# Optimization experiments

Hardware: AMD Instinct MI355X
Metric: run time of the kernel (lower is better)

The kernel has to match this reference:

```python
import jax, jax.numpy as jnp
import numpy as np

MARGIN = 0.1  # init kwarg: margin
# type_of_distance='euclidean', type_of_quadruplets='hard', what_is_hard='one'


def _distance_euclidean(x):
    # l2-normalize rows, then all-pairs euclidean distance (torch.cdist p=2)
    x = x / jnp.linalg.norm(x, axis=1, keepdims=True)
    sq = jnp.sum(x * x, axis=1)
    d2 = sq[:, None] + sq[None, :] - 2.0 * (x @ x.T)
    return jnp.sqrt(jnp.maximum(d2, 0.0))


def setup_inputs() -> dict:
    key = jax.random.key(0)
    k1, k2 = jax.random.split(key)
    B, D, C = 256, 512, 80
    logits = jax.random.normal(k1, (B, D), dtype=jnp.float32)
    # sparse multi-hot labels: ~2.4 active classes per sample
    labels = (jax.random.uniform(k2, (B, C)) < 0.03).astype(jnp.float32)
    return {"logits": logits, "labels": labels}


def reference(logits, labels):
    n = labels.shape[0]
    sames = (labels @ labels.T) > 0                      # [B,B] bool
    diffs = ~sames
    sames = sames & ~jnp.eye(n, dtype=bool)              # fill_diagonal_(0)
    triu = jnp.triu(jnp.ones((n, n), dtype=bool), k=1)   # J < K
    # O(B^3) quadruplet-candidate mask: sames[I,J] & sames[I,K] & (J<K)
    mask = sames[:, :, None] & sames[:, None, :] & triu[None, :, :]
    I, J, K = jnp.nonzero(mask)                          # row-major, same as torch.where
    # expand each (I,J,K) triplet with every negative N of anchor I
    rows, cols = jnp.nonzero(diffs[I])                   # [n_quads]
    quadruplets = jnp.stack([I[rows], J[rows], K[rows], cols], axis=1)

    mat = _distance_euclidean(jax.lax.stop_gradient(logits))  # logits.detach()
    Ii, Jj, Kk, Nn = quadruplets[:, 0], quadruplets[:, 1], quadruplets[:, 2], quadruplets[:, 3]
    ij = mat[Ii, Jj]
    ik = mat[Ii, Kk]
    innd = mat[Ii, Nn]
    m1 = innd - ij
    m2 = innd - ik
    # type_of_quadruplets='hard', what_is_hard='one' (opt = OR)
    cond = ((m1 <= MARGIN) | (m2 <= MARGIN)) & ((m1 <= 0) | (m2 <= 0))
    return quadruplets[cond]
```

## Files before the change

### kernel.cpp

```cpp
#include <hip/hip_runtime.h>
#include <math.h>

#define NB 256
#define ND 512
#define NC 80
#define NSPLIT 8
#define SLOT 32640
#define KW_WAVES (NB * NSPLIT * 4)

__device__ float g_x [NB * ND];
__device__ float g_xt[ND * NB];
__device__ float g_sq[NB];
__device__ float g_ddneg[NB * NB];
__device__ unsigned long long g_m[NB * 2];
__device__ int   g_atot[NB];
__device__ int   g_abase[NB];
__device__ int   g_cursor;
__device__ int4  g_trip[NB * SLOT];

__device__ __forceinline__ int block_scan_int(int val, int* wsum) {
    int tid = threadIdx.x, wv = tid >> 6, ln = tid & 63;
    int v = val;
    #pragma unroll
    for (int off = 1; off < 64; off <<= 1) {
        int u = __shfl_up(v, off);
        v += (ln >= off) ? u : 0;
    }
    __syncthreads();
    if (ln == 63) wsum[wv] = v;
    __syncthreads();
    int add = 0;
    #pragma unroll
    for (int w = 0; w < 4; ++w) if (w < wv) add += wsum[w];
    return v + add;
}

__device__ __forceinline__ int ubcount(const float* s, float thr) {
    int pos = 0;
    #pragma unroll
    for (int step = 128; step > 0; step >>= 1) {
        int np = pos + step;
        if (s[np - 1] <= thr) pos = np;
    }
    return pos;
}

__global__ __launch_bounds__(256) void k_prep(const float* __restrict__ logits,
                                              const float* __restrict__ labels) {
    int b = blockIdx.x, tid = threadIdx.x;
    __shared__ double red[NB];
    if (b == 0 && tid == 0) g_cursor = 0;
    float v0 = logits[b * ND + tid];
    float v1 = logits[b * ND + 256 + tid];
    red[tid] = (double)(v0 * v0) + (double)(v1 * v1);
    __syncthreads();
    for (int off = 128; off > 0; off >>= 1) {
        if (tid < off) red[tid] += red[tid + off];
        __syncthreads();
    }
    float S = (float)red[0];
    float nrm = sqrtf(S);
    __syncthreads();
    float a0 = v0 / nrm;
    float a1 = v1 / nrm;
    g_x[b * ND + tid]          = a0;
    g_x[b * ND + 256 + tid]    = a1;
    g_xt[tid * NB + b]         = a0;
    g_xt[(tid + 256) * NB + b] = a1;
    red[tid] = (double)(a0 * a0) + (double)(a1 * a1);
    __syncthreads();
    for (int off = 128; off > 0; off >>= 1) {
        if (tid < off) red[tid] += red[tid + off];
        __syncthreads();
    }
    if (tid == 0) g_sq[b] = (float)red[0];
    int wv = tid >> 6, ln = tid & 63;
    if (wv == 0) {
        unsigned long long m0 = __ballot(labels[b * NC + ln] != 0.0f);
        if (ln == 0) g_m[2 * b] = m0;
    } else if (wv == 1) {
        bool p = (ln < 16) ? (labels[b * NC + 64 + ln] != 0.0f) : false;
        unsigned long long m1 = __ballot(p);
        if (ln == 0) g_m[2 * b + 1] = m1;
    }
}

__global__ __launch_bounds__(256) void k_count() {
    __shared__ float xi[ND];
    __shared__ float s_dd[NB], s_sort[NB];
    __shared__ int s_w4[4], s_rowbase[NB], s_base;
    __shared__ short s_plist[NB];
    int i = blockIdx.x, tid = threadIdx.x;
    xi[tid]       = g_x[i * ND + tid];
    xi[tid + 256] = g_x[i * ND + 256 + tid];
    __syncthreads();
    double dot = 0.0;
    #pragma unroll 8
    for (int c = 0; c < ND; ++c)
        dot = fma((double)xi[c], (double)g_xt[c * NB + tid], dot);
    float dotf = (float)dot;
    float sm   = g_sq[i] + g_sq[tid];
    float d2   = sm - 2.0f * dotf;
    float dv   = sqrtf(d2 > 0.0f ? d2 : 0.0f);
    s_dd[tid] = dv;
    unsigned long long mi0 = g_m[2 * i],   mi1 = g_m[2 * i + 1];
    unsigned long long mt0 = g_m[2 * tid], mt1 = g_m[2 * tid + 1];
    bool shl   = ((mi0 & mt0) | (mi1 & mt1)) != 0ULL;
    bool isPos = shl && (tid != i);
    float ddneg = shl ? INFINITY : dv;
    g_ddneg[i * NB + tid] = ddneg;
    int incl = block_scan_int(isPos ? 1 : 0, s_w4);
    int P = s_w4[0] + s_w4[1] + s_w4[2] + s_w4[3];
    if (isPos) s_plist[incl - 1] = (short)tid;
    if (tid < P - 1) s_rowbase[tid] = tid * (P - 1) - (tid * (tid - 1)) / 2;
    float v = ddneg;
    for (int k = 2; k <= 256; k <<= 1)
        for (int j = k >> 1; j > 0; j >>= 1) {
            float oth;
            if (j >= 64) {
                __syncthreads();
                s_sort[tid] = v;
                __syncthreads();
                oth = s_sort[tid ^ j];
            } else {
                oth = __shfl_xor(v, j);
            }
            bool keepmin = (((tid & k) == 0) == ((tid & j) == 0));
            v = keepmin ? fminf(v, oth) : fmaxf(v, oth);
        }
    __syncthreads();
    s_sort[tid] = v;
    int T = P * (P - 1) / 2;
    if (tid == 0) s_base = (T > 0) ? atomicAdd(&g_cursor, T) : 0;
    __syncthreads();
    int dbase = s_base;
    int carried = 0;
    for (int cb = 0; cb < T; cb += NB) {
        int t = cb + tid;
        int cnt = 0, jk = 0;
        float thr = 0.0f;
        if (t < T) {
            int a = 0;
            #pragma unroll
            for (int step = 128; step > 0; step >>= 1) {
                int na = a + step;
                if (na <= P - 2 && s_rowbase[na] <= t) a = na;
            }
            int b = a + 1 + (t - s_rowbase[a]);
            int jj = s_plist[a], kk = s_plist[b];
            thr = fmaxf(s_dd[jj], s_dd[kk]);
            jk  = jj | (kk << 8);
            cnt = ubcount(s_sort, thr);
        }
        int inc2 = block_scan_int(cnt, s_w4);
        int chunkTot = s_w4[0] + s_w4[1] + s_w4[2] + s_w4[3];
        if (t < T)
            g_trip[dbase + t] =
                make_int4(jk, __float_as_int(thr), carried + inc2 - cnt, i);
        carried += chunkTot;
    }
    if (tid == 0) g_atot[i] = carried;
}

__global__ __launch_bounds__(256) void k_abase() {
    __shared__ int s_w4[4];
    int tid = threadIdx.x;
    int v = g_atot[tid];
    int incl = block_scan_int(v, s_w4);
    g_abase[tid] = incl - v;
}

__global__ __launch_bounds__(256) void k_write(int4* __restrict__ out, int maxQuads) {
    int tid = threadIdx.x;
    int wv = tid >> 6, ln = tid & 63;
    int W = (blockIdx.x << 2) | wv;
    int Ttot = g_cursor;
    unsigned long long lanemask = (1ULL << ln) - 1ULL;
    int t = W;
    int4 tr = (t < Ttot) ? g_trip[t] : make_int4(0, 0, 0, 0);
    while (t < Ttot) {
        int tn = t + KW_WAVES;
        int4 nxt = (tn < Ttot) ? g_trip[tn] : make_int4(0, 0, 0, 0);
        int ai = tr.w;
        const float* row = g_ddneg + ai * NB;
        float v0 = row[ln], v1 = row[64 + ln];
        float v2 = row[128 + ln], v3 = row[192 + ln];
        int base = g_abase[ai] + tr.z;
        int jj = tr.x & 255, kk = tr.x >> 8;
        float thr = __int_as_float(tr.y);
        bool f0 = (v0 <= thr), f1 = (v1 <= thr);
        bool f2 = (v2 <= thr), f3 = (v3 <= thr);
        unsigned long long m0 = __ballot(f0), m1 = __ballot(f1);
        unsigned long long m2 = __ballot(f2), m3 = __ballot(f3);
        int b1 = base + __popcll(m0);
        int b2 = b1 + __popcll(m1);
        int b3 = b2 + __popcll(m2);
        if (f0) { int pos = base + __popcll(m0 & lanemask);
                  if (pos < maxQuads) out[pos] = make_int4(ai, jj, kk, ln); }
        if (f1) { int pos = b1 + __popcll(m1 & lanemask);
                  if (pos < maxQuads) out[pos] = make_int4(ai, jj, kk, 64 | ln); }
        if (f2) { int pos = b2 + __popcll(m2 & lanemask);
                  if (pos < maxQuads) out[pos] = make_int4(ai, jj, kk, 128 | ln); }
        if (f3) { int pos = b3 + __popcll(m3 & lanemask);
                  if (pos < maxQuads) out[pos] = make_int4(ai, jj, kk, 192 | ln); }
        tr = nxt;
        t = tn;
    }
}

extern "C" void kernel_launch(void* const* d_in, const int* in_sizes, int n_in,
                              void* d_out, int out_size, void* d_ws, size_t ws_size,
                              hipStream_t stream) {
    const float* logits = (const float*)d_in[0];
    const float* labels = (const float*)d_in[1];
    if (n_in >= 2 && in_sizes[0] == NB * NC && in_sizes[1] == NB * ND) {
        logits = (const float*)d_in[1];
        labels = (const float*)d_in[0];
    }
    int maxQuads = out_size / 4;

    k_prep <<<NB, NB, 0, stream>>>(logits, labels);
    k_count<<<NB, NB, 0, stream>>>();
    k_abase<<<1,  NB, 0, stream>>>();
    k_write<<<NB * NSPLIT, NB, 0, stream>>>((int4*)d_out, maxQuads);
}
```

Baseline: 187.2 us.

## Fuse anchor-base scan into write kernel and process contiguous triplet chunks per wave

Removes the separate k_abase launch: each k_write block redoes the 256-entry prefix scan of per-anchor totals into shared memory. Each wave now takes a contiguous range of triplets instead of a strided one. It loads 64 triplets with one coalesced read and broadcasts them via shuffles, and reloads the anchor's negative-distance row only when the anchor changes. This cuts a launch, redundant row loads and scattered triplet reads. The cost is a redundant scan in every block and more serialized per-triplet work inside each wave.

New measurement: 185.6 us. No clear change (-0.9%).

```diff
diff --git a/kernel.cpp b/kernel.cpp
--- a/kernel.cpp
+++ b/kernel.cpp
@@ -14,7 +14,6 @@
 __device__ float g_ddneg[NB * NB];
 __device__ unsigned long long g_m[NB * 2];
 __device__ int   g_atot[NB];
-__device__ int   g_abase[NB];
 __device__ int   g_cursor;
 __device__ int4  g_trip[NB * SLOT];
 
@@ -162,49 +161,62 @@
     if (tid == 0) g_atot[i] = carried;
 }
 
-__global__ __launch_bounds__(256) void k_abase() {
+__global__ __launch_bounds__(256) void k_write(int4* __restrict__ out, int maxQuads) {
     __shared__ int s_w4[4];
+    __shared__ int s_abase[NB];
     int tid = threadIdx.x;
-    int v = g_atot[tid];
-    int incl = block_scan_int(v, s_w4);
-    g_abase[tid] = incl - v;
-}
-
-__global__ __launch_bounds__(256) void k_write(int4* __restrict__ out, int maxQuads) {
-    int tid = threadIdx.x;
+    int av = g_atot[tid];
+    int incl = block_scan_int(av, s_w4);
+    s_abase[tid] = incl - av;
+    __syncthreads();
+
     int wv = tid >> 6, ln = tid & 63;
     int W = (blockIdx.x << 2) | wv;
     int Ttot = g_cursor;
+    int per = (Ttot + KW_WAVES - 1) / KW_WAVES;
+    int t0 = W * per;
+    if (t0 >= Ttot) return;
+    int t1 = t0 + per; if (t1 > Ttot) t1 = Ttot;
     unsigned long long lanemask = (1ULL << ln) - 1ULL;
-    int t = W;
-    int4 tr = (t < Ttot) ? g_trip[t] : make_int4(0, 0, 0, 0);
-    while (t < Ttot) {
-        int tn = t + KW_WAVES;
-        int4 nxt = (tn < Ttot) ? g_trip[tn] : make_int4(0, 0, 0, 0);
-        int ai = tr.w;
-        const float* row = g_ddneg + ai * NB;
-        float v0 = row[ln], v1 = row[64 + ln];
-        float v2 = row[128 + ln], v3 = row[192 + ln];
-        int base = g_abase[ai] + tr.z;
-        int jj = tr.x & 255, kk = tr.x >> 8;
-        float thr = __int_as_float(tr.y);
-        bool f0 = (v0 <= thr), f1 = (v1 <= thr);
-        bool f2 = (v2 <= thr), f3 = (v3 <= thr);
-        unsigned long long m0 = __ballot(f0), m1 = __ballot(f1);
-        unsigned long long m2 = __ballot(f2), m3 = __ballot(f3);
-        int b1 = base + __popcll(m0);
-        int b2 = b1 + __popcll(m1);
-        int b3 = b2 + __popcll(m2);
-        if (f0) { int pos = base + __popcll(m0 & lanemask);
-                  if (pos < maxQuads) out[pos] = make_int4(ai, jj, kk, ln); }
-        if (f1) { int pos = b1 + __popcll(m1 & lanemask);
-                  if (pos < maxQuads) out[pos] = make_int4(ai, jj, kk, 64 | ln); }
-        if (f2) { int pos = b2 + __popcll(m2 & lanemask);
-                  if (pos < maxQuads) out[pos] = make_int4(ai, jj, kk, 128 | ln); }
-        if (f3) { int pos = b3 + __popcll(m3 & lanemask);
-                  if (pos < maxQuads) out[pos] = make_int4(ai, jj, kk, 192 | ln); }
-        tr = nxt;
-        t = tn;
+
+    int cur_ai = -1;
+    int base_a = 0;
+    float v0 = 0.0f, v1 = 0.0f, v2 = 0.0f, v3 = 0.0f;
+
+    for (int tb = t0; tb < t1; tb += 64) {
+        int nk = t1 - tb; if (nk > 64) nk = 64;
+        int4 myTr = (tb + ln < t1) ? g_trip[tb + ln] : make_int4(0, 0, 0, 0);
+        for (int k = 0; k < nk; ++k) {
+            int jk   = __shfl(myTr.x, k);
+            int thri = __shfl(myTr.y, k);
+            int toff = __shfl(myTr.z, k);
+            int ai   = __shfl(myTr.w, k);
+            if (ai != cur_ai) {
+                const float* row = g_ddneg + ai * NB;
+                v0 = row[ln];       v1 = row[64 + ln];
+                v2 = row[128 + ln]; v3 = row[192 + ln];
+                base_a = s_abase[ai];
+                cur_ai = ai;
+            }
+            float thr = __int_as_float(thri);
+            int base = base_a + toff;
+            int jj = jk & 255, kk = jk >> 8;
+            bool f0 = (v0 <= thr), f1 = (v1 <= thr);
+            bool f2 = (v2 <= thr), f3 = (v3 <= thr);
+            unsigned long long m0 = __ballot(f0), m1 = __ballot(f1);
+            unsigned long long m2 = __ballot(f2), m3 = __ballot(f3);
+            int b1 = base + __popcll(m0);
+            int b2 = b1 + __popcll(m1);
+            int b3 = b2 + __popcll(m2);
+            if (f0) { int pos = base + __popcll(m0 & lanemask);
+                      if (pos < maxQuads) out[pos] = make_int4(ai, jj, kk, ln); }
+            if (f1) { int pos = b1 + __popcll(m1 & lanemask);
+                      if (pos < maxQuads) out[pos] = make_int4(ai, jj, kk, 64 | ln); }
+            if (f2) { int pos = b2 + __popcll(m2 & lanemask);
+                      if (pos < maxQuads) out[pos] = make_int4(ai, jj, kk, 128 | ln); }
+            if (f3) { int pos = b3 + __popcll(m3 & lanemask);
+                      if (pos < maxQuads) out[pos] = make_int4(ai, jj, kk, 192 | ln); }
+        }
     }
 }
 
@@ -221,6 +233,5 @@
 
     k_prep <<<NB, NB, 0, stream>>>(logits, labels);
     k_count<<<NB, NB, 0, stream>>>();
-    k_abase<<<1,  NB, 0, stream>>>();
     k_write<<<NB * NSPLIT, NB, 0, stream>>>((int4*)d_out, maxQuads);
 }
```
